# Kernel optimization log

Measured on AMD Instinct MI355X. Metric: run time of the kernel, lower is better.

The kernel has to match this reference:

```python
import jax, jax.numpy as jnp
import numpy as np

B, N = 2, 8192
D_POINTS, D_MODEL, K = 64, 128, 16


def _lin(key, fi, fo):
    return jax.random.normal(key, (fi, fo), jnp.float32) / np.sqrt(fi)


def setup_inputs() -> dict:
    key = jax.random.key(0)
    ks = jax.random.split(key, 16)
    return {
        "xyz": jax.random.normal(ks[0], (B, N, 3), jnp.float32),
        "normals": jax.random.normal(ks[1], (B, N, 3), jnp.float32),
        "features": jax.random.normal(ks[2], (B, N, D_POINTS), jnp.float32),
        "fc1_w": _lin(ks[3], D_POINTS, D_MODEL), "fc1_b": jnp.zeros((D_MODEL,), jnp.float32),
        "fc2_w": _lin(ks[4], D_MODEL, D_POINTS), "fc2_b": jnp.zeros((D_POINTS,), jnp.float32),
        "gamma_w1": _lin(ks[5], D_MODEL, D_MODEL), "gamma_b1": jnp.zeros((D_MODEL,), jnp.float32),
        "gamma_w2": _lin(ks[6], D_MODEL, D_MODEL), "gamma_b2": jnp.zeros((D_MODEL,), jnp.float32),
        "delta_w1": _lin(ks[7], 3, D_MODEL), "delta_b1": jnp.zeros((D_MODEL,), jnp.float32),
        "delta_w2": _lin(ks[8], D_MODEL, D_MODEL), "delta_b2": jnp.zeros((D_MODEL,), jnp.float32),
        "wq": _lin(ks[9], D_MODEL, D_MODEL),
        "wk": _lin(ks[10], D_MODEL, D_MODEL),
        "wv": _lin(ks[11], D_MODEL, D_MODEL),
    }


def _gather(points, idx):
    # points: (b, n, c), idx: (b, n, k) -> (b, n, k, c)
    b, n, c = points.shape
    k = idx.shape[-1]
    flat = jnp.take_along_axis(points, idx.reshape(b, n * k, 1), axis=1)
    return flat.reshape(b, n, k, c)


def reference(xyz, normals, features, fc1_w, fc1_b, fc2_w, fc2_b,
              gamma_w1, gamma_b1, gamma_w2, gamma_b2,
              delta_w1, delta_b1, delta_w2, delta_b2, wq, wk, wv):
    # pairwise squared distances (b, n, n)
    sq = jnp.sum(xyz * xyz, axis=-1)
    dists = sq[:, :, None] + sq[:, None, :] - 2.0 * jnp.einsum('bnd,bmd->bnm', xyz, xyz)
    _, knn_idx = jax.lax.top_k(-dists, K)  # k smallest distances (includes self)

    knn_xyz = _gather(xyz, knn_idx)                      # (b, n, k, 3)
    x = features @ fc1_w + fc1_b                         # (b, n, d_model)
    q = x @ wq                                           # (b, n, d_model)
    k_nbr = _gather(x @ wk, knn_idx)                     # (b, n, k, d_model)
    v_nbr = _gather(x @ wv, knn_idx)                     # (b, n, k, d_model)

    # positional encoding: fc_delta(rel_pos), ends with ReLU
    rel = xyz[:, :, None, :] - knn_xyz                   # (b, n, k, 3)
    pos_enc = jax.nn.relu(jax.nn.relu(rel @ delta_w1 + delta_b1) @ delta_w2 + delta_b2)

    # vector attention logits: fc_gamma(q - k + pos_enc)
    h = q[:, :, None, :] - k_nbr + pos_enc
    logits = jax.nn.relu(h @ gamma_w1 + gamma_b1) @ gamma_w2 + gamma_b2
    attn = jax.nn.softmax(logits / np.sqrt(D_MODEL), axis=-2)  # softmax over neighbors

    res = jnp.einsum('bnkf,bnkf->bnf', attn, v_nbr + pos_enc)
    res = res @ fc2_w + fc2_b + features
    return res, attn
```

## Files before the change

kernel.cpp:

```cpp
#include <hip/hip_runtime.h>
#include <cstdint>

typedef unsigned long long ull;
typedef __bf16 bf16x8 __attribute__((ext_vector_type(8)));
typedef float f32x4 __attribute__((ext_vector_type(4)));

#define NPTS 8192
#define NB 2
#define KNN 16
#define DM 128
#define PADK 136

__device__ __forceinline__ float sq3f(float x, float y, float z) {
    return __fadd_rn(__fadd_rn(__fmul_rn(x, x), __fmul_rn(y, y)), __fmul_rn(z, z));
}
__device__ __forceinline__ float dot3f(float ax, float ay, float az, float bx, float by, float bz) {
    return __fadd_rn(__fadd_rn(__fmul_rn(ax, bx), __fmul_rn(ay, by)), __fmul_rn(az, bz));
}
__device__ __forceinline__ unsigned ford(unsigned u) {
    return (u & 0x80000000u) ? ~u : (u | 0x80000000u);
}
__device__ __forceinline__ float inv_ford(unsigned f) {
    unsigned u = (f & 0x80000000u) ? (f ^ 0x80000000u) : ~f;
    return __uint_as_float(u);
}

__global__ __launch_bounds__(256) void knn_kernel(const float* __restrict__ xyz,
                                                  int* __restrict__ idx_out) {
    __shared__ float4 xs4[1024];
    const int t = threadIdx.x;
    const int wv = t >> 6, lane = t & 63;
    const int q_id = blockIdx.x * 4 + wv;
    const int b = q_id >> 13;
    const int i = q_id & (NPTS - 1);
    const float* xb = xyz + (size_t)b * NPTS * 3;
    const float qx = xb[3 * i + 0], qy = xb[3 * i + 1], qz = xb[3 * i + 2];
    const float sqi = sq3f(qx, qy, qz);

    unsigned list_hi = 0xffffffffu, list_lo = 0xffffffffu;
    float thrF = __uint_as_float(0x7f800000u);

    for (int ch = 0; ch < 8; ++ch) {
        __syncthreads();
#pragma unroll
        for (int e = 0; e < 4; e++) {
            int p = t + e * 256;
            int g = ch * 1024 + p;
            float x = xb[3 * g + 0], y = xb[3 * g + 1], z = xb[3 * g + 2];
            xs4[p] = make_float4(x, y, z, sq3f(x, y, z));
        }
        __syncthreads();
        for (int m = 0; m < 8; m++) {
            const int jl = m * 128 + lane;
            float4 P = xs4[jl];
            float4 Q = xs4[jl + 64];
            float dA = __fsub_rn(__fadd_rn(sqi, P.w),
                                 __fmul_rn(2.0f, dot3f(qx, qy, qz, P.x, P.y, P.z)));
            float dB = __fsub_rn(__fadd_rn(sqi, Q.w),
                                 __fmul_rn(2.0f, dot3f(qx, qy, qz, Q.x, Q.y, Q.z)));
            bool ta = (dA <= thrF), tb = (dB <= thrF);
            ull ballot = __ballot(ta || tb);
            if (ballot == 0ull) continue;
            const unsigned jbase = (unsigned)(ch * 1024 + m * 128);
            do {
                int l = (int)__builtin_ctzll(ballot);
                ballot &= ballot - 1;
                float fA = __uint_as_float(
                    (unsigned)__builtin_amdgcn_readlane(__float_as_int(dA), l));
                float fB = __uint_as_float(
                    (unsigned)__builtin_amdgcn_readlane(__float_as_int(dB), l));
#pragma unroll
                for (int half = 0; half < 2; half++) {
                    float fc = half ? fB : fA;
                    if (fc <= thrF) {
                        unsigned ck_hi = ford(__float_as_uint(fc));
                        unsigned ck_lo = jbase + (unsigned)l + (half ? 64u : 0u);
                        unsigned ph = __shfl_up(list_hi, 1);
                        unsigned pl = __shfl_up(list_lo, 1);
                        bool lt = (ck_hi < list_hi) || (ck_hi == list_hi && ck_lo < list_lo);
                        bool ge = (lane == 0) || (ck_hi > ph) || (ck_hi == ph && ck_lo >= pl);
                        unsigned nh = ge ? ck_hi : ph;
                        unsigned nl = ge ? ck_lo : pl;
                        list_hi = lt ? nh : list_hi;
                        list_lo = lt ? nl : list_lo;
                        unsigned th = (unsigned)__builtin_amdgcn_readlane((int)list_hi, 15);
                        th = (th > 0xff800000u) ? 0xff800000u : th;
                        thrF = inv_ford(th);
                    }
                }
            } while (ballot);
        }
    }
    if (lane < 16)
        idx_out[q_id * 16 + lane] = (int)list_lo;
}

__global__ __launch_bounds__(256) void wprep_kernel(const float* __restrict__ d2,
                                                    const float* __restrict__ g1,
                                                    const float* __restrict__ g2,
                                                    __bf16* __restrict__ d2t,
                                                    __bf16* __restrict__ g1t,
                                                    __bf16* __restrict__ g2t) {
    const float* src = (blockIdx.x == 0) ? d2 : ((blockIdx.x == 1) ? g1 : g2);
    __bf16* dst = (blockIdx.x == 0) ? d2t : ((blockIdx.x == 1) ? g1t : g2t);
#pragma unroll
    for (int e = 0; e < 64; e++) {
        int id = threadIdx.x + e * 256;
        int k = id >> 7, n = id & 127;
        dst[n * 128 + k] = (__bf16)src[id];
    }
}

__global__ __launch_bounds__(256, 1) void gemm_x_kernel(const float* __restrict__ feats,
                                                        const float* __restrict__ w,
                                                        const float* __restrict__ bias,
                                                        float* __restrict__ xout) {
    __shared__ float At[64 * 65];
    __shared__ __align__(16) float Wt[64 * 128];
    const int t = threadIdx.x;
    const int base = blockIdx.x * 64;
#pragma unroll
    for (int e = 0; e < 16; e++) {
        int id = t + e * 256;
        int r = id >> 6, c = id & 63;
        At[c * 65 + r] = feats[(size_t)(base + r) * 64 + c];
    }
#pragma unroll
    for (int e = 0; e < 32; e++) { int id = t + e * 256; Wt[id] = w[id]; }
    __syncthreads();
    const int r0 = (t >> 4) * 4;
    const int c0 = (t & 15) * 8;
    float acc[4][8];
#pragma unroll
    for (int i = 0; i < 4; i++)
#pragma unroll
        for (int j = 0; j < 8; j++) acc[i][j] = bias[c0 + j];
#pragma unroll 4
    for (int kk = 0; kk < 64; ++kk) {
        float a0 = At[kk * 65 + r0 + 0];
        float a1 = At[kk * 65 + r0 + 1];
        float a2 = At[kk * 65 + r0 + 2];
        float a3 = At[kk * 65 + r0 + 3];
        const float4 w0 = *(const float4*)&Wt[kk * 128 + c0];
        const float4 w1 = *(const float4*)&Wt[kk * 128 + c0 + 4];
        float wj[8] = {w0.x, w0.y, w0.z, w0.w, w1.x, w1.y, w1.z, w1.w};
#pragma unroll
        for (int j = 0; j < 8; j++) {
            acc[0][j] += a0 * wj[j];
            acc[1][j] += a1 * wj[j];
            acc[2][j] += a2 * wj[j];
            acc[3][j] += a3 * wj[j];
        }
    }
#pragma unroll
    for (int i = 0; i < 4; i++)
#pragma unroll
        for (int j = 0; j < 8; j++)
            xout[(size_t)(base + r0 + i) * 128 + c0 + j] = acc[i][j];
}

__global__ __launch_bounds__(256, 1) void gemm_qkv_kernel(const float* __restrict__ x,
                                                          const float* __restrict__ wq,
                                                          const float* __restrict__ wk,
                                                          const float* __restrict__ wv,
                                                          float* __restrict__ qo,
                                                          float* __restrict__ ko,
                                                          float* __restrict__ vo) {
    const float* w = (blockIdx.y == 0) ? wq : ((blockIdx.y == 1) ? wk : wv);
    float* o = (blockIdx.y == 0) ? qo : ((blockIdx.y == 1) ? ko : vo);
    __shared__ float At[128 * 65];
    __shared__ __align__(16) float Wt[128 * 128];
    const int t = threadIdx.x;
    const int base = blockIdx.x * 64;
#pragma unroll
    for (int e = 0; e < 32; e++) {
        int id = t + e * 256;
        int r = id >> 7, c = id & 127;
        At[c * 65 + r] = x[(size_t)(base + r) * 128 + c];
    }
#pragma unroll
    for (int e = 0; e < 64; e++) { int id = t + e * 256; Wt[id] = w[id]; }
    __syncthreads();
    const int r0 = (t >> 4) * 4;
    const int c0 = (t & 15) * 8;
    float acc[4][8];
#pragma unroll
    for (int i = 0; i < 4; i++)
#pragma unroll
        for (int j = 0; j < 8; j++) acc[i][j] = 0.0f;
#pragma unroll 4
    for (int kk = 0; kk < 128; ++kk) {
        float a0 = At[kk * 65 + r0 + 0];
        float a1 = At[kk * 65 + r0 + 1];
        float a2 = At[kk * 65 + r0 + 2];
        float a3 = At[kk * 65 + r0 + 3];
        const float4 w0 = *(const float4*)&Wt[kk * 128 + c0];
        const float4 w1 = *(const float4*)&Wt[kk * 128 + c0 + 4];
        float wj[8] = {w0.x, w0.y, w0.z, w0.w, w1.x, w1.y, w1.z, w1.w};
#pragma unroll
        for (int j = 0; j < 8; j++) {
            acc[0][j] += a0 * wj[j];
            acc[1][j] += a1 * wj[j];
            acc[2][j] += a2 * wj[j];
            acc[3][j] += a3 * wj[j];
        }
    }
#pragma unroll
    for (int i = 0; i < 4; i++)
#pragma unroll
        for (int j = 0; j < 8; j++)
            o[(size_t)(base + r0 + i) * 128 + c0 + j] = acc[i][j];
}

#define DO_GEMM(ACC0, ACC1, WPTR)                                                          \
    {                                                                                      \
        _Pragma("unroll")                                                                  \
        for (int kt = 0; kt < 4; kt++) {                                                   \
            const int ko = kt * 32 + 8 * lg;                                               \
            bf16x8 a0 = *(const bf16x8*)&Ab[(rbase + lr) * PADK + ko];                     \
            bf16x8 a1 = *(const bf16x8*)&Ab[(rbase + 16 + lr) * PADK + ko];                \
            _Pragma("unroll")                                                              \
            for (int ct = 0; ct < 8; ct++) {                                               \
                bf16x8 bv = *(const bf16x8*)&WPTR[(ct * 16 + lr) * PADK + ko];             \
                ACC0[ct] = __builtin_amdgcn_mfma_f32_16x16x32_bf16(a0, bv, ACC0[ct], 0, 0, 0); \
                ACC1[ct] = __builtin_amdgcn_mfma_f32_16x16x32_bf16(a1, bv, ACC1[ct], 0, 0, 0); \
            }                                                                              \
        }                                                                                  \
    }

#define STAGE_W(SRC)                                                                       \
    {                                                                                      \
        _Pragma("unroll")                                                                  \
        for (int e = 0; e < 8; e++) {                                                      \
            int ch = t + e * 256;                                                          \
            int r = ch >> 4, ck = ch & 15;                                                 \
            *(bf16x8*)&Wb[r * PADK + ck * 8] = *(const bf16x8*)&SRC[r * 128 + ck * 8];     \
        }                                                                                  \
    }

__global__ __launch_bounds__(256, 2) void k345_kernel(const float* __restrict__ xyz,
                                                      const int* __restrict__ idxw,
                                                      const float* __restrict__ q,
                                                      const float* __restrict__ xk,
                                                      const float* __restrict__ xv,
                                                      const float* __restrict__ d1,
                                                      const float* __restrict__ bd1,
                                                      const float* __restrict__ bd2,
                                                      const float* __restrict__ bg1,
                                                      const float* __restrict__ bg2,
                                                      const __bf16* __restrict__ d2t,
                                                      const __bf16* __restrict__ g1t,
                                                      const __bf16* __restrict__ g2t,
                                                      float* __restrict__ attn,
                                                      float* __restrict__ res_pre) {
    __shared__ __bf16 Ab[128 * PADK];
    __shared__ __bf16 Wb[128 * PADK];
    __shared__ float rels[128 * 4];
    __shared__ int jrow[128];
    __shared__ float d1s[3 * 128];
    __shared__ float bd1s[128], bd2s[128], bg1s[128], bg2s[128];

    const int t = threadIdx.x;
    const int wv = t >> 6;
    const int lane = t & 63;
    const int lr = lane & 15, lg = lane >> 4;
    const int R0 = blockIdx.x * 128;
    const int b = R0 >> 17;
    const int rbase = wv * 32;

#pragma unroll
    for (int e = 0; e < 2; e++) { int id = t + e * 256; if (id < 384) d1s[id] = d1[id]; }
    if (t < 128) {
        bd1s[t] = bd1[t]; bd2s[t] = bd2[t]; bg1s[t] = bg1[t]; bg2s[t] = bg2[t];
    } else {
        int r = t - 128;
        int j = idxw[R0 + r];
        jrow[r] = j;
        const float* pn = xyz + (size_t)((R0 + r) >> 4) * 3;
        const float* pj = xyz + (size_t)((b << 13) + j) * 3;
        rels[r * 4 + 0] = pn[0] - pj[0];
        rels[r * 4 + 1] = pn[1] - pj[1];
        rels[r * 4 + 2] = pn[2] - pj[2];
    }
    STAGE_W(d2t)
    __syncthreads();

    {
        const int c = t & 127;
        const float w0 = d1s[c], w1 = d1s[128 + c], w2 = d1s[256 + c], bb = bd1s[c];
#pragma unroll
        for (int e = 0; e < 64; e++) {
            int r = (t >> 7) + e * 2;
            float v = fmaf(rels[r * 4 + 2], w2,
                      fmaf(rels[r * 4 + 1], w1, fmaf(rels[r * 4 + 0], w0, bb)));
            Ab[r * PADK + c] = (__bf16)fmaxf(v, 0.0f);
        }
    }
    __syncthreads();

    f32x4 acc0[8], acc1[8];
#pragma unroll
    for (int ct = 0; ct < 8; ct++) {
        float bb = bd2s[ct * 16 + lr];
        acc0[ct] = (f32x4){bb, bb, bb, bb};
        acc1[ct] = acc0[ct];
    }
    DO_GEMM(acc0, acc1, Wb)
    f32x4 pos0[8], pos1[8];
#pragma unroll
    for (int ct = 0; ct < 8; ct++) {
#pragma unroll
        for (int e = 0; e < 4; e++) {
            pos0[ct][e] = fmaxf(acc0[ct][e], 0.0f);
            pos1[ct][e] = fmaxf(acc1[ct][e], 0.0f);
        }
    }

#pragma unroll
    for (int rt = 0; rt < 2; rt++) {
        const int rloc = rbase + rt * 16 + 4 * lg;
        const size_t qbase = (size_t)((R0 + rloc) >> 4) * 128;
        const int j0 = jrow[rloc + 0], j1 = jrow[rloc + 1];
        const int j2 = jrow[rloc + 2], j3 = jrow[rloc + 3];
        const size_t kb0 = (size_t)((b << 13) + j0) * 128;
        const size_t kb1 = (size_t)((b << 13) + j1) * 128;
        const size_t kb2 = (size_t)((b << 13) + j2) * 128;
        const size_t kb3 = (size_t)((b << 13) + j3) * 128;
        f32x4* posR = rt ? pos1 : pos0;
#pragma unroll
        for (int ct = 0; ct < 8; ct++) {
            const int c = ct * 16 + lr;
            const float qv = q[qbase + c];
            f32x4 p = posR[ct];
            Ab[(rloc + 0) * PADK + c] = (__bf16)(p[0] + qv - xk[kb0 + c]);
            Ab[(rloc + 1) * PADK + c] = (__bf16)(p[1] + qv - xk[kb1 + c]);
            Ab[(rloc + 2) * PADK + c] = (__bf16)(p[2] + qv - xk[kb2 + c]);
            Ab[(rloc + 3) * PADK + c] = (__bf16)(p[3] + qv - xk[kb3 + c]);
        }
    }
    __syncthreads();
    STAGE_W(g1t)
    __syncthreads();

#pragma unroll
    for (int ct = 0; ct < 8; ct++) {
        float bb = bg1s[ct * 16 + lr];
        acc0[ct] = (f32x4){bb, bb, bb, bb};
        acc1[ct] = acc0[ct];
    }
    DO_GEMM(acc0, acc1, Wb)
#pragma unroll
    for (int rt = 0; rt < 2; rt++) {
        const int rloc = rbase + rt * 16 + 4 * lg;
        f32x4* accR = rt ? acc1 : acc0;
#pragma unroll
        for (int ct = 0; ct < 8; ct++) {
            const int c = ct * 16 + lr;
            f32x4 p = accR[ct];
            Ab[(rloc + 0) * PADK + c] = (__bf16)fmaxf(p[0], 0.0f);
            Ab[(rloc + 1) * PADK + c] = (__bf16)fmaxf(p[1], 0.0f);
            Ab[(rloc + 2) * PADK + c] = (__bf16)fmaxf(p[2], 0.0f);
            Ab[(rloc + 3) * PADK + c] = (__bf16)fmaxf(p[3], 0.0f);
        }
    }
    __syncthreads();
    STAGE_W(g2t)
    __syncthreads();

#pragma unroll
    for (int ct = 0; ct < 8; ct++) {
        float bb = bg2s[ct * 16 + lr];
        acc0[ct] = (f32x4){bb, bb, bb, bb};
        acc1[ct] = acc0[ct];
    }
    DO_GEMM(acc0, acc1, Wb)
    const float scale = 0.08838834764831845f;
#pragma unroll
    for (int rt = 0; rt < 2; rt++) {
        const int rloc = rbase + rt * 16 + 4 * lg;
        const int j0 = jrow[rloc + 0], j1 = jrow[rloc + 1];
        const int j2 = jrow[rloc + 2], j3 = jrow[rloc + 3];
        const size_t vb0 = (size_t)((b << 13) + j0) * 128;
        const size_t vb1 = (size_t)((b << 13) + j1) * 128;
        const size_t vb2 = (size_t)((b << 13) + j2) * 128;
        const size_t vb3 = (size_t)((b << 13) + j3) * 128;
        f32x4* accR = rt ? acc1 : acc0;
        f32x4* posR = rt ? pos1 : pos0;
#pragma unroll
        for (int ct = 0; ct < 8; ct++) {
            const int c = ct * 16 + lr;
            f32x4 p = accR[ct];
            float l0 = p[0] * scale, l1 = p[1] * scale, l2 = p[2] * scale, l3 = p[3] * scale;
            float m = fmaxf(fmaxf(l0, l1), fmaxf(l2, l3));
            m = fmaxf(m, __shfl_xor(m, 16));
            m = fmaxf(m, __shfl_xor(m, 32));
            float e0 = __expf(l0 - m), e1 = __expf(l1 - m);
            float e2 = __expf(l2 - m), e3 = __expf(l3 - m);
            float s = (e0 + e1) + (e2 + e3);
            s += __shfl_xor(s, 16);
            s += __shfl_xor(s, 32);
            float inv = 1.0f / s;
            float a0 = e0 * inv, a1 = e1 * inv, a2 = e2 * inv, a3 = e3 * inv;
            size_t ob = (size_t)(R0 + rloc) * 128 + c;
            attn[ob + 0 * 128] = a0;
            attn[ob + 1 * 128] = a1;
            attn[ob + 2 * 128] = a2;
            attn[ob + 3 * 128] = a3;
            f32x4 pp = posR[ct];
            float r = a0 * (xv[vb0 + c] + pp[0])
                    + a1 * (xv[vb1 + c] + pp[1])
                    + a2 * (xv[vb2 + c] + pp[2])
                    + a3 * (xv[vb3 + c] + pp[3]);
            r += __shfl_xor(r, 16);
            r += __shfl_xor(r, 32);
            if (lg == 0)
                res_pre[(size_t)((R0 >> 4) + wv * 2 + rt) * 128 + c] = r;
        }
    }
}

__global__ __launch_bounds__(256, 1) void k6_kernel(const float* __restrict__ res_pre,
                                                    const float* __restrict__ w,
                                                    const float* __restrict__ bias,
                                                    const float* __restrict__ feats,
                                                    float* __restrict__ res_out) {
    __shared__ float At[128 * 65];
    __shared__ __align__(16) float Wt[128 * 64];
    const int t = threadIdx.x;
    const int base = blockIdx.x * 64;
#pragma unroll
    for (int e = 0; e < 32; e++) {
        int id = t + e * 256;
        int r = id >> 7, c = id & 127;
        At[c * 65 + r] = res_pre[(size_t)(base + r) * 128 + c];
    }
#pragma unroll
    for (int e = 0; e < 32; e++) { int id = t + e * 256; Wt[id] = w[id]; }
    __syncthreads();
    const int r0 = (t >> 4) * 4;
    const int c0 = (t & 15) * 4;
    float acc[4][4];
#pragma unroll
    for (int i = 0; i < 4; i++)
#pragma unroll
        for (int j = 0; j < 4; j++) acc[i][j] = bias[c0 + j];
#pragma unroll 4
    for (int kk = 0; kk < 128; ++kk) {
        float a0 = At[kk * 65 + r0 + 0];
        float a1 = At[kk * 65 + r0 + 1];
        float a2 = At[kk * 65 + r0 + 2];
        float a3 = At[kk * 65 + r0 + 3];
        const float4 w0 = *(const float4*)&Wt[kk * 64 + c0];
        float wj[4] = {w0.x, w0.y, w0.z, w0.w};
#pragma unroll
        for (int j = 0; j < 4; j++) {
            acc[0][j] += a0 * wj[j];
            acc[1][j] += a1 * wj[j];
            acc[2][j] += a2 * wj[j];
            acc[3][j] += a3 * wj[j];
        }
    }
#pragma unroll
    for (int i = 0; i < 4; i++)
#pragma unroll
        for (int j = 0; j < 4; j++)
            res_out[(size_t)(base + r0 + i) * 64 + c0 + j] =
                acc[i][j] + feats[(size_t)(base + r0 + i) * 64 + c0 + j];
}

extern "C" void kernel_launch(void* const* d_in, const int* in_sizes, int n_in,
                              void* d_out, int out_size, void* d_ws, size_t ws_size,
                              hipStream_t stream) {
    (void)in_sizes; (void)n_in; (void)out_size; (void)ws_size;
    const float* xyz   = (const float*)d_in[0];
    const float* feats = (const float*)d_in[2];
    const float* fc1_w = (const float*)d_in[3];
    const float* fc1_b = (const float*)d_in[4];
    const float* fc2_w = (const float*)d_in[5];
    const float* fc2_b = (const float*)d_in[6];
    const float* g1    = (const float*)d_in[7];
    const float* bg1   = (const float*)d_in[8];
    const float* g2    = (const float*)d_in[9];
    const float* bg2   = (const float*)d_in[10];
    const float* d1    = (const float*)d_in[11];
    const float* bd1   = (const float*)d_in[12];
    const float* d2    = (const float*)d_in[13];
    const float* bd2   = (const float*)d_in[14];
    const float* wq    = (const float*)d_in[15];
    const float* wk    = (const float*)d_in[16];
    const float* wv    = (const float*)d_in[17];

    int* idxw   = (int*)d_ws;
    float* xbuf = (float*)((char*)d_ws + (1 << 20));
    float* qbuf = xbuf + 2097152;
    float* kbuf = qbuf + 2097152;
    float* vbuf = kbuf + 2097152;
    float* rpre = vbuf + 2097152;
    __bf16* d2t = (__bf16*)(rpre + 2097152);
    __bf16* g1t = d2t + 16384;
    __bf16* g2t = g1t + 16384;

    float* res_out = (float*)d_out;
    float* attn    = res_out + 1048576;

    wprep_kernel<<<3, 256, 0, stream>>>(d2, g1, g2, d2t, g1t, g2t);
    knn_kernel<<<4096, 256, 0, stream>>>(xyz, idxw);
    gemm_x_kernel<<<256, 256, 0, stream>>>(feats, fc1_w, fc1_b, xbuf);
    gemm_qkv_kernel<<<dim3(256, 3), 256, 0, stream>>>(xbuf, wq, wk, wv, qbuf, kbuf, vbuf);
    k345_kernel<<<2048, 256, 0, stream>>>(xyz, idxw, qbuf, kbuf, vbuf, d1, bd1, bd2, bg1, bg2,
                                          d2t, g1t, g2t, attn, rpre);
    k6_kernel<<<256, 256, 0, stream>>>(rpre, fc2_w, fc2_b, feats, res_out);
}
```

Baseline: 285.9 us.

## Seed kNN threshold from first tile and fuse x/qkv GEMMs with bf16 MFMA

The kNN kernel now seeds its distance threshold from the first 128 candidates (the max over 16 groups of per-group minima, which guarantees at least 16 candidates fall at or below it). This prunes early insertions, and candidates are processed as separate A and B ballots. The fc1 GEMM and the q/k/v projections are fused into one kernel that keeps x in LDS as bf16 and runs the three projections with MFMA instead of scalar FP32, removing the x round trip through global memory and one launch. The change trades q/k/v precision (bf16 inputs) for tensor-core throughput, and the seeded threshold relies on the 16-of-128 bound for correctness.

New measurement: 244.4 us (median of 2 runs). -14.5%, faster.

```diff
diff --git a/kernel.cpp b/kernel.cpp
--- a/kernel.cpp
+++ b/kernel.cpp
@@ -40,6 +40,21 @@
     unsigned list_hi = 0xffffffffu, list_lo = 0xffffffffu;
     float thrF = __uint_as_float(0x7f800000u);
 
+#define INSERT(FC, CKLO)                                                                 \
+    {                                                                                    \
+        unsigned ck_hi = ford(__float_as_uint(FC));                                      \
+        unsigned ck_lo = (CKLO);                                                         \
+        unsigned ph = __shfl_up(list_hi, 1);                                             \
+        unsigned pl = __shfl_up(list_lo, 1);                                             \
+        bool lt = (ck_hi < list_hi) || (ck_hi == list_hi && ck_lo < list_lo);            \
+        bool ge = (lane == 0) || (ck_hi > ph) || (ck_hi == ph && ck_lo >= pl);           \
+        list_hi = lt ? (ge ? ck_hi : ph) : list_hi;                                      \
+        list_lo = lt ? (ge ? ck_lo : pl) : list_lo;                                      \
+        unsigned th = (unsigned)__builtin_amdgcn_readlane((int)list_hi, 15);             \
+        th = (th > 0xff800000u) ? 0xff800000u : th;            \
+        thrF = fminf(thrF, inv_ford(th));                                                \
+    }
+
     for (int ch = 0; ch < 8; ++ch) {
         __syncthreads();
 #pragma unroll
@@ -58,39 +73,38 @@
                                  __fmul_rn(2.0f, dot3f(qx, qy, qz, P.x, P.y, P.z)));
             float dB = __fsub_rn(__fadd_rn(sqi, Q.w),
                                  __fmul_rn(2.0f, dot3f(qx, qy, qz, Q.x, Q.y, Q.z)));
-            bool ta = (dA <= thrF), tb = (dB <= thrF);
-            ull ballot = __ballot(ta || tb);
-            if (ballot == 0ull) continue;
+            if (ch == 0 && m == 0) {
+                float mn = fminf(dA, dB);
+                mn = fminf(mn, __shfl_xor(mn, 1));
+                mn = fminf(mn, __shfl_xor(mn, 2));
+                float mx = mn;
+                mx = fmaxf(mx, __shfl_xor(mx, 4));
+                mx = fmaxf(mx, __shfl_xor(mx, 8));
+                mx = fmaxf(mx, __shfl_xor(mx, 16));
+                mx = fmaxf(mx, __shfl_xor(mx, 32));
+                thrF = mx;
+            }
+            ull balA = __ballot(dA <= thrF);
+            ull balB = __ballot(dB <= thrF);
+            if ((balA | balB) == 0ull) continue;
             const unsigned jbase = (unsigned)(ch * 1024 + m * 128);
-            do {
-                int l = (int)__builtin_ctzll(ballot);
-                ballot &= ballot - 1;
-                float fA = __uint_as_float(
+            while (balA) {
+                int l = (int)__builtin_ctzll(balA);
+                balA &= balA - 1;
+                float fc = __uint_as_float(
                     (unsigned)__builtin_amdgcn_readlane(__float_as_int(dA), l));
-                float fB = __uint_as_float(
+                if (fc <= thrF) INSERT(fc, jbase + (unsigned)l)
+            }
+            while (balB) {
+                int l = (int)__builtin_ctzll(balB);
+                balB &= balB - 1;
+                float fc = __uint_as_float(
                     (unsigned)__builtin_amdgcn_readlane(__float_as_int(dB), l));
-#pragma unroll
-                for (int half = 0; half < 2; half++) {
-                    float fc = half ? fB : fA;
-                    if (fc <= thrF) {
-                        unsigned ck_hi = ford(__float_as_uint(fc));
-                        unsigned ck_lo = jbase + (unsigned)l + (half ? 64u : 0u);
-                        unsigned ph = __shfl_up(list_hi, 1);
-                        unsigned pl = __shfl_up(list_lo, 1);
-                        bool lt = (ck_hi < list_hi) || (ck_hi == list_hi && ck_lo < list_lo);
-                        bool ge = (lane == 0) || (ck_hi > ph) || (ck_hi == ph && ck_lo >= pl);
-                        unsigned nh = ge ? ck_hi : ph;
-                        unsigned nl = ge ? ck_lo : pl;
-                        list_hi = lt ? nh : list_hi;
-                        list_lo = lt ? nl : list_lo;
-                        unsigned th = (unsigned)__builtin_amdgcn_readlane((int)list_hi, 15);
-                        th = (th > 0xff800000u) ? 0xff800000u : th;
-                        thrF = inv_ford(th);
-                    }
-                }
-            } while (ballot);
-        }
-    }
+                if (fc <= thrF) INSERT(fc, jbase + 64u + (unsigned)l)
+            }
+        }
+    }
+#undef INSERT
     if (lane < 16)
         idx_out[q_id * 16 + lane] = (int)list_lo;
 }
@@ -98,11 +112,20 @@
 __global__ __launch_bounds__(256) void wprep_kernel(const float* __restrict__ d2,
                                                     const float* __restrict__ g1,
                                                     const float* __restrict__ g2,
+                                                    const float* __restrict__ wq,
+                                                    const float* __restrict__ wk,
+                                                    const float* __restrict__ wv,
                                                     __bf16* __restrict__ d2t,
                                                     __bf16* __restrict__ g1t,
-                                                    __bf16* __restrict__ g2t) {
-    const float* src = (blockIdx.x == 0) ? d2 : ((blockIdx.x == 1) ? g1 : g2);
-    __bf16* dst = (blockIdx.x == 0) ? d2t : ((blockIdx.x == 1) ? g1t : g2t);
+                                                    __bf16* __restrict__ g2t,
+                                                    __bf16* __restrict__ wqt,
+                                                    __bf16* __restrict__ wkt,
+                                                    __bf16* __restrict__ wvt) {
+    const int bi = blockIdx.x;
+    const float* src = (bi == 0) ? d2 : (bi == 1) ? g1 : (bi == 2) ? g2
+                     : (bi == 3) ? wq : (bi == 4) ? wk : wv;
+    __bf16* dst = (bi == 0) ? d2t : (bi == 1) ? g1t : (bi == 2) ? g2t
+                : (bi == 3) ? wqt : (bi == 4) ? wkt : wvt;
 #pragma unroll
     for (int e = 0; e < 64; e++) {
         int id = threadIdx.x + e * 256;
@@ -111,14 +134,33 @@
     }
 }
 
-__global__ __launch_bounds__(256, 1) void gemm_x_kernel(const float* __restrict__ feats,
-                                                        const float* __restrict__ w,
-                                                        const float* __restrict__ bias,
-                                                        float* __restrict__ xout) {
-    __shared__ float At[64 * 65];
-    __shared__ __align__(16) float Wt[64 * 128];
+#define STAGE_W(SRC)                                                                       \
+    {                                                                                      \
+        _Pragma("unroll")                                                                  \
+        for (int e = 0; e < 8; e++) {                                                      \
+            int ch = t + e * 256;                                                          \
+            int r = ch >> 4, ck = ch & 15;                                                 \
+            *(bf16x8*)&Wb[r * PADK + ck * 8] = *(const bf16x8*)&SRC[r * 128 + ck * 8];     \
+        }                                                                                  \
+    }
+
+__global__ __launch_bounds__(256, 1) void xqkv_kernel(const float* __restrict__ feats,
+                                                      const float* __restrict__ fc1_w,
+                                                      const float* __restrict__ fc1_b,
+                                                      const __bf16* __restrict__ wqt,
+                                                      const __bf16* __restrict__ wkt,
+                                                      const __bf16* __restrict__ wvt,
+                                                      float* __restrict__ qo,
+                                                      float* __restrict__ ko,
+                                                      float* __restrict__ vo) {
+    __shared__ __align__(16) char lds[52224];
+    float* At = (float*)lds;
+    float* Wt = (float*)(lds + 16640);
+    __bf16* Ab = (__bf16*)lds;
+    __bf16* Wb = (__bf16*)(lds + 17408);
     const int t = threadIdx.x;
     const int base = blockIdx.x * 64;
+
 #pragma unroll
     for (int e = 0; e < 16; e++) {
         int id = t + e * 256;
@@ -126,7 +168,7 @@
         At[c * 65 + r] = feats[(size_t)(base + r) * 64 + c];
     }
 #pragma unroll
-    for (int e = 0; e < 32; e++) { int id = t + e * 256; Wt[id] = w[id]; }
+    for (int e = 0; e < 32; e++) { int id = t + e * 256; Wt[id] = fc1_w[id]; }
     __syncthreads();
     const int r0 = (t >> 4) * 4;
     const int c0 = (t & 15) * 8;
@@ -134,7 +176,7 @@
 #pragma unroll
     for (int i = 0; i < 4; i++)
 #pragma unroll
-        for (int j = 0; j < 8; j++) acc[i][j] = bias[c0 + j];
+        for (int j = 0; j < 8; j++) acc[i][j] = fc1_b[c0 + j];
 #pragma unroll 4
     for (int kk = 0; kk < 64; ++kk) {
         float a0 = At[kk * 65 + r0 + 0];
@@ -152,64 +194,52 @@
             acc[3][j] += a3 * wj[j];
         }
     }
+    __syncthreads();
+
 #pragma unroll
     for (int i = 0; i < 4; i++)
 #pragma unroll
         for (int j = 0; j < 8; j++)
-            xout[(size_t)(base + r0 + i) * 128 + c0 + j] = acc[i][j];
-}
-
-__global__ __launch_bounds__(256, 1) void gemm_qkv_kernel(const float* __restrict__ x,
-                                                          const float* __restrict__ wq,
-                                                          const float* __restrict__ wk,
-                                                          const float* __restrict__ wv,
-                                                          float* __restrict__ qo,
-                                                          float* __restrict__ ko,
-                                                          float* __restrict__ vo) {
-    const float* w = (blockIdx.y == 0) ? wq : ((blockIdx.y == 1) ? wk : wv);
-    float* o = (blockIdx.y == 0) ? qo : ((blockIdx.y == 1) ? ko : vo);
-    __shared__ float At[128 * 65];
-    __shared__ __align__(16) float Wt[128 * 128];
-    const int t = threadIdx.x;
-    const int base = blockIdx.x * 64;
-#pragma unroll
-    for (int e = 0; e < 32; e++) {
-        int id = t + e * 256;
-        int r = id >> 7, c = id & 127;
-        At[c * 65 + r] = x[(size_t)(base + r) * 128 + c];
-    }
-#pragma unroll
-    for (int e = 0; e < 64; e++) { int id = t + e * 256; Wt[id] = w[id]; }
-    __syncthreads();
-    const int r0 = (t >> 4) * 4;
-    const int c0 = (t & 15) * 8;
-    float acc[4][8];
-#pragma unroll
-    for (int i = 0; i < 4; i++)
-#pragma unroll
-        for (int j = 0; j < 8; j++) acc[i][j] = 0.0f;
-#pragma unroll 4
-    for (int kk = 0; kk < 128; ++kk) {
-        float a0 = At[kk * 65 + r0 + 0];
-        float a1 = At[kk * 65 + r0 + 1];
-        float a2 = At[kk * 65 + r0 + 2];
-        float a3 = At[kk * 65 + r0 + 3];
-        const float4 w0 = *(const float4*)&Wt[kk * 128 + c0];
-        const float4 w1 = *(const float4*)&Wt[kk * 128 + c0 + 4];
-        float wj[8] = {w0.x, w0.y, w0.z, w0.w, w1.x, w1.y, w1.z, w1.w};
-#pragma unroll
-        for (int j = 0; j < 8; j++) {
-            acc[0][j] += a0 * wj[j];
-            acc[1][j] += a1 * wj[j];
-            acc[2][j] += a2 * wj[j];
-            acc[3][j] += a3 * wj[j];
-        }
-    }
-#pragma unroll
-    for (int i = 0; i < 4; i++)
-#pragma unroll
-        for (int j = 0; j < 8; j++)
-            o[(size_t)(base + r0 + i) * 128 + c0 + j] = acc[i][j];
+            Ab[(r0 + i) * PADK + c0 + j] = (__bf16)acc[i][j];
+    STAGE_W(wqt)
+    __syncthreads();
+
+    const int lane = t & 63;
+    const int lr = lane & 15, lg = lane >> 4;
+    const int rbase = (t >> 6) * 16;
+
+#define QGEMM(ACC, OUT)                                                                    \
+    {                                                                                      \
+        f32x4 ACC[8];                                                                      \
+        _Pragma("unroll")                                                                  \
+        for (int ct = 0; ct < 8; ct++) ACC[ct] = (f32x4){0.f, 0.f, 0.f, 0.f};              \
+        _Pragma("unroll")                                                                  \
+        for (int kt = 0; kt < 4; kt++) {                                                   \
+            const int ko = kt * 32 + 8 * lg;                                               \
+            bf16x8 a0 = *(const bf16x8*)&Ab[(rbase + lr) * PADK + ko];                     \
+            _Pragma("unroll")                                                              \
+            for (int ct = 0; ct < 8; ct++) {                                               \
+                bf16x8 bv = *(const bf16x8*)&Wb[(ct * 16 + lr) * PADK + ko];               \
+                ACC[ct] = __builtin_amdgcn_mfma_f32_16x16x32_bf16(a0, bv, ACC[ct], 0, 0, 0); \
+            }                                                                              \
+        }                                                                                  \
+        _Pragma("unroll")                                                                  \
+        for (int ct = 0; ct < 8; ct++)                                                     \
+            _Pragma("unroll")                                                              \
+            for (int e = 0; e < 4; e++)                                                    \
+                OUT[(size_t)(base + rbase + 4 * lg + e) * 128 + ct * 16 + lr] = ACC[ct][e]; \
+    }
+
+    QGEMM(accq, qo)
+    __syncthreads();
+    STAGE_W(wkt)
+    __syncthreads();
+    QGEMM(acck, ko)
+    __syncthreads();
+    STAGE_W(wvt)
+    __syncthreads();
+    QGEMM(accv, vo)
+#undef QGEMM
 }
 
 #define DO_GEMM(ACC0, ACC1, WPTR)                                                          \
@@ -225,16 +255,6 @@
                 ACC0[ct] = __builtin_amdgcn_mfma_f32_16x16x32_bf16(a0, bv, ACC0[ct], 0, 0, 0); \
                 ACC1[ct] = __builtin_amdgcn_mfma_f32_16x16x32_bf16(a1, bv, ACC1[ct], 0, 0, 0); \
             }                                                                              \
-        }                                                                                  \
-    }
-
-#define STAGE_W(SRC)                                                                       \
-    {                                                                                      \
-        _Pragma("unroll")                                                                  \
-        for (int e = 0; e < 8; e++) {                                                      \
-            int ch = t + e * 256;                                                          \
-            int r = ch >> 4, ck = ch & 15;                                                 \
-            *(bf16x8*)&Wb[r * PADK + ck * 8] = *(const bf16x8*)&SRC[r * 128 + ck * 8];     \
         }                                                                                  \
     }
 
@@ -491,22 +511,25 @@
     const float* wv    = (const float*)d_in[17];
 
     int* idxw   = (int*)d_ws;
-    float* xbuf = (float*)((char*)d_ws + (1 << 20));
-    float* qbuf = xbuf + 2097152;
+    float* qbuf = (float*)((char*)d_ws + (1 << 20));
     float* kbuf = qbuf + 2097152;
     float* vbuf = kbuf + 2097152;
     float* rpre = vbuf + 2097152;
     __bf16* d2t = (__bf16*)(rpre + 2097152);
     __bf16* g1t = d2t + 16384;
     __bf16* g2t = g1t + 16384;
+    __bf16* wqt = g2t + 16384;
+    __bf16* wkt = wqt + 16384;
+    __bf16* wvt = wkt + 16384;
 
     float* res_out = (float*)d_out;
     float* attn    = res_out + 1048576;
 
-    wprep_kernel<<<3, 256, 0, stream>>>(d2, g1, g2, d2t, g1t, g2t);
+    wprep_kernel<<<6, 256, 0, stream>>>(d2, g1, g2, wq, wk, wv,
+                                        d2t, g1t, g2t, wqt, wkt, wvt);
     knn_kernel<<<4096, 256, 0, stream>>>(xyz, idxw);
-    gemm_x_kernel<<<256, 256, 0, stream>>>(feats, fc1_w, fc1_b, xbuf);
-    gemm_qkv_kernel<<<dim3(256, 3), 256, 0, stream>>>(xbuf, wq, wk, wv, qbuf, kbuf, vbuf);
+    xqkv_kernel<<<256, 256, 0, stream>>>(feats, fc1_w, fc1_b, wqt, wkt, wvt,
+                                         qbuf, kbuf, vbuf);
     k345_kernel<<<2048, 256, 0, stream>>>(xyz, idxw, qbuf, kbuf, vbuf, d1, bd1, bd2, bg1, bg2,
                                           d2t, g1t, g2t, attn, rpre);
     k6_kernel<<<256, 256, 0, stream>>>(rpre, fc2_w, fc2_b, feats, res_out);
```
